# Performance work log

Hardware: AMD Instinct MI355X
Metric: run time of the kernel (lower is better)

Reference implementation:

```python
import jax, jax.numpy as jnp
import numpy as np

RADIUS = 0.1
NSAMPLE = 32
EPS = 1e-5


def ball_query(radius, nsample, xyz):
    # xyz: [B, N, 3] -> idx [B, N, nsample] (query set == support set)
    B, N, _ = xyz.shape
    # pairwise squared distances [B, N, N]
    sq = jnp.sum((xyz[:, :, None, :] - xyz[:, None, :, :]) ** 2, axis=-1)
    grp = jnp.broadcast_to(jnp.arange(N, dtype=jnp.int32), (B, N, N))
    grp = jnp.where(sq > radius * radius, N, grp)
    grp = jnp.sort(grp, axis=-1)[:, :, :nsample]
    first = grp[:, :, 0:1]
    return jnp.where(grp == N, first, grp)  # self is always in-ball -> first valid


def index_points(points, idx):
    # points [B, N, C], idx [B, N, S] -> [B, N, S, C]
    B, N, S = idx.shape
    C = points.shape[-1]
    flat = jnp.take_along_axis(points, idx.reshape(B, N * S, 1), axis=1)
    return flat.reshape(B, N, S, C)


def bn(x, gamma, beta, mean, var, axis):
    # eval-mode batchnorm over channel axis
    shape = [1] * x.ndim
    shape[axis] = -1
    g = gamma.reshape(shape); b = beta.reshape(shape)
    m = mean.reshape(shape); v = var.reshape(shape)
    return (x - m) * (g * jax.lax.rsqrt(v + EPS)) + b


def setup_inputs() -> dict:
    key = jax.random.key(0)
    ks = jax.random.split(key, 8)
    B, N, C, E = 4, 4096, 128, 4
    H = C * E
    xyz = jax.random.uniform(ks[0], (B, N, 3), dtype=jnp.float32)
    feats = jax.random.normal(ks[1], (B, N, C), dtype=jnp.float32)
    s = 0.05
    Wn = jax.random.normal(ks[2], (C, C + 3), dtype=jnp.float32) * s
    W1 = jax.random.normal(ks[3], (H, C), dtype=jnp.float32) * s
    W2 = jax.random.normal(ks[4], (C, H), dtype=jnp.float32) * s
    def bnp(k, n):
        k1, k2 = jax.random.split(k)
        return (jnp.ones((n,), jnp.float32) + 0.01 * jax.random.normal(k1, (n,)),
                0.01 * jax.random.normal(k2, (n,)),
                jnp.zeros((n,), jnp.float32),
                jnp.ones((n,), jnp.float32))
    gn, bn_, mn, vn = bnp(ks[5], C)
    g1, b1, m1, v1 = bnp(ks[6], H)
    g2, b2, m2, v2 = bnp(ks[7], C)
    return dict(xyz=xyz, feats=feats, Wn=Wn, gn=gn, bn_=bn_, mn=mn, vn=vn,
                W1=W1, g1=g1, b1=b1, m1=m1, v1=v1,
                W2=W2, g2=g2, b2=b2, m2=m2, v2=v2)


def reference(xyz, feats, Wn, gn, bn_, mn, vn, W1, g1, b1, m1, v1, W2, g2, b2, m2, v2):
    B, N, C = feats.shape
    identity = feats  # [B, N, C]
    idx = ball_query(RADIUS, NSAMPLE, xyz)  # [B, N, S]
    grouped_xyz = index_points(xyz, idx) - xyz[:, :, None, :]  # [B, N, S, 3]
    grouped_xyz = grouped_xyz / RADIUS  # normalize_dp
    grouped_feats = index_points(feats, idx)  # [B, N, S, C]
    grouped = jnp.concatenate([grouped_xyz, grouped_feats], axis=-1)  # [B, N, S, C+3]
    # torch layout [B, C+3, S, N]; keep [B, N, S, C+3] and contract channels
    x = jnp.einsum('oc,bnsc->bnso', Wn, grouped)  # neighbor 1x1 conv
    x = jax.nn.relu(bn(x, gn, bn_, mn, vn, axis=3))
    x = jnp.max(x, axis=2)  # max over neighbors -> [B, N, C]
    # inverted bottleneck pointwise MLP
    h = jnp.einsum('hc,bnc->bnh', W1, x)
    h = jax.nn.relu(bn(h, g1, b1, m1, v1, axis=2))
    y = jnp.einsum('ch,bnh->bnc', W2, h)
    y = bn(y, g2, b2, m2, v2, axis=2)
    out = jax.nn.relu(y + identity)  # [B, N, C]
    return out
```

## Files before the change

### kernel.cpp

```cpp
#include <hip/hip_runtime.h>
#include <hip/hip_bf16.h>
#include <math.h>

static constexpr int BB = 4;
static constexpr int NN = 4096;
static constexpr int CC = 128;
static constexpr int HH = 512;
static constexpr int SS = 32;
static constexpr float EPSF = 1e-5f;
static constexpr int NCELL = 1000;

typedef __bf16 bf16_t;
typedef bf16_t bf16x8 __attribute__((ext_vector_type(8)));
typedef float f32x4 __attribute__((ext_vector_type(4)));
typedef float f32x2 __attribute__((ext_vector_type(2)));

__device__ inline unsigned short f2bf(float f) {
    unsigned int u = __builtin_bit_cast(unsigned int, f);
    u += 0x7FFFu + ((u >> 16) & 1u);
    return (unsigned short)(u >> 16);
}
__device__ inline float bf2f(unsigned short s) {
    unsigned int u = ((unsigned int)s) << 16;
    return __builtin_bit_cast(float, u);
}
__device__ inline float u2f(unsigned int u) {
    return __builtin_bit_cast(float, u);
}
__device__ inline int cell_of(float v) {
    int c = (int)(v * 10.0f);
    return c > 9 ? 9 : (c < 0 ? 0 : c);
}
__device__ inline f32x2 pk_fma_b(f32x2 a, float g, f32x2 c) {
    const f32x2 gg = {g, g};
    return a * gg + c;
}

__device__ inline void gload_lds16(const void* g, void* l) {
    __builtin_amdgcn_global_load_lds(
        (const __attribute__((address_space(1))) unsigned int*)g,
        (__attribute__((address_space(3))) unsigned int*)l, 16, 0, 0);
}

__global__ __launch_bounds__(256)
void prep_kernel(const float* __restrict__ Wn, const float* __restrict__ W1,
                 const float* __restrict__ W2, const float* __restrict__ feats,
                 const float* __restrict__ gn, const float* __restrict__ bnv,
                 const float* __restrict__ mn, const float* __restrict__ vn,
                 unsigned short* __restrict__ WnF, unsigned short* __restrict__ W1b,
                 unsigned short* __restrict__ W2b, unsigned short* __restrict__ featsb,
                 int* __restrict__ counts, float4* __restrict__ wfold)
{
    const int blk = blockIdx.x;
    const int t   = threadIdx.x;
    if (blk < 576) {
        const int i = blk * 256 + t;
        if (i < 16384) {
            const int o = i >> 7, c = i & 127;
            WnF[i] = f2bf(Wn[o * 131 + 3 + c]);
        } else if (i < 16384 + 65536) {
            const int k = i - 16384;
            W1b[k] = f2bf(W1[k]);
        } else if (i < 16384 + 131072) {
            const int k = i - 16384 - 65536;
            W2b[k] = f2bf(W2[k]);
        }
    } else if (blk < 2624) {
        const int i = (blk - 576) * 256 + t;
        const float4 v = ((const float4*)feats)[i];
        unsigned long long pk = (unsigned long long)f2bf(v.x)
                              | ((unsigned long long)f2bf(v.y) << 16)
                              | ((unsigned long long)f2bf(v.z) << 32)
                              | ((unsigned long long)f2bf(v.w) << 48);
        ((unsigned long long*)featsb)[i] = pk;
    } else if (blk < 2640) {
        const int i = (blk - 2624) * 256 + t;
        if (i < BB * NCELL) counts[i] = 0;
    } else {
        if (t < CC) {
            const float sc = gn[t] / sqrtf(vn[t] + EPSF);
            wfold[t] = make_float4(sc * Wn[t * 131 + 0], sc * Wn[t * 131 + 1],
                                   sc * Wn[t * 131 + 2], bnv[t] - mn[t] * sc);
        }
    }
}

__global__ __launch_bounds__(256)
void count_kernel(const float* __restrict__ xyz, int* __restrict__ counts)
{
    const int p = blockIdx.x * 256 + threadIdx.x;
    const int b = p >> 12;
    const float x = xyz[p * 3 + 0], y = xyz[p * 3 + 1], z = xyz[p * 3 + 2];
    const int cid = cell_of(z) * 100 + cell_of(y) * 10 + cell_of(x);
    atomicAdd(&counts[b * NCELL + cid], 1);
}

__global__ __launch_bounds__(1024)
void scan_kernel(const int* __restrict__ counts, int* __restrict__ starts,
                 int* __restrict__ cursor)
{
    const int t  = threadIdx.x;
    const int i0 = t * 4;
    int v[4];
    #pragma unroll
    for (int k = 0; k < 4; ++k)
        v[k] = (i0 + k < BB * NCELL) ? counts[i0 + k] : 0;
    const int s = v[0] + v[1] + v[2] + v[3];

    __shared__ int ls[1024];
    ls[t] = s;
    __syncthreads();
    #pragma unroll
    for (int off = 1; off < 1024; off <<= 1) {
        const int add = (t >= off) ? ls[t - off] : 0;
        __syncthreads();
        ls[t] += add;
        __syncthreads();
    }
    int ex = ls[t] - s;
    #pragma unroll
    for (int k = 0; k < 4; ++k) {
        if (i0 + k < BB * NCELL) {
            starts[i0 + k] = ex;
            cursor[i0 + k] = ex;
        }
        ex += v[k];
    }
    if (t == 1023) starts[BB * NCELL] = ls[1023];
}

__global__ __launch_bounds__(256)
void scatter_kernel(const float* __restrict__ xyz, int* __restrict__ cursor,
                    float4* __restrict__ spts)
{
    const int p = blockIdx.x * 256 + threadIdx.x;
    const int b = p >> 12;
    const int n = p & (NN - 1);
    const float x = xyz[p * 3 + 0], y = xyz[p * 3 + 1], z = xyz[p * 3 + 2];
    const int cid = cell_of(z) * 100 + cell_of(y) * 10 + cell_of(x);
    const int pos = atomicAdd(&cursor[b * NCELL + cid], 1);
    spts[pos] = make_float4(x, y, z, __int_as_float(n));
}

__global__ __launch_bounds__(64)
void ball_query_binned_kernel(const float* __restrict__ xyz,
                              const int* __restrict__ starts,
                              const float4* __restrict__ spts,
                              int* __restrict__ idx)
{
    const int p    = blockIdx.x;
    const int b    = p >> 12;
    const int lane = threadIdx.x;

    const float qx = xyz[p * 3 + 0];
    const float qy = xyz[p * 3 + 1];
    const float qz = xyz[p * 3 + 2];
    const int cx = cell_of(qx), cy = cell_of(qy), cz = cell_of(qz);
    const int xlo = cx > 0 ? cx - 1 : 0;
    const int xhi = cx < 9 ? cx + 1 : 9;

    __shared__ int list[128];
    __shared__ int res[SS];
    int cnt = 0;

    for (int dz = -1; dz <= 1; ++dz) {
        const int z2 = cz + dz;
        if (z2 < 0 || z2 > 9) continue;
        for (int dy = -1; dy <= 1; ++dy) {
            const int y2 = cy + dy;
            if (y2 < 0 || y2 > 9) continue;
            const int base = b * NCELL + z2 * 100 + y2 * 10;
            const int lo = starts[base + xlo];
            const int hi = starts[base + xhi + 1];
            for (int j0 = lo; j0 < hi; j0 += 64) {
                const int j = j0 + lane;
                bool in = false;
                int pi = 0;
                if (j < hi) {
                    const float4 s = spts[j];
                    float sq;
                    {
                        #pragma clang fp contract(off)
                        const float dx  = qx - s.x;
                        const float dyv = qy - s.y;
                        const float dzv = qz - s.z;
                        sq = dx * dx + dyv * dyv + dzv * dzv;
                    }
                    in = (sq <= 0.01f);
                    pi = __float_as_int(s.w);
                }
                const unsigned long long mask = __ballot(in);
                if (in) {
                    const int pos = cnt + __popcll(mask & ((1ull << lane) - 1ull));
                    if (pos < 128) list[pos] = pi;
                }
                cnt += (int)__popcll(mask);
            }
        }
    }
    __syncthreads();

    const int c = cnt < 128 ? cnt : 128;
    #pragma unroll
    for (int l0 = 0; l0 < 2; ++l0) {
        const int l = lane + l0 * 64;
        if (l < c) {
            const int v = list[l];
            int r = 0;
            for (int k = 0; k < c; ++k) r += (list[k] < v);
            if (r < SS) res[r] = v;
        }
    }
    __syncthreads();

    if (lane < SS) {
        const int m = c < SS ? c : SS;
        idx[(size_t)p * SS + lane] = (lane < m) ? res[lane] : res[0];
    }
}

__global__ __launch_bounds__(256)
void group_max_kernel(const float* __restrict__ xyz,
                      const unsigned short* __restrict__ T,
                      const float4* __restrict__ wfold,
                      const int* __restrict__ idx, unsigned short* __restrict__ xout)
{
    const int t   = threadIdx.x;
    const int ptl = t >> 5;
    const int l   = t & 31;
    const int p   = blockIdx.x * 8 + ptl;
    const int b   = p >> 12;

    __shared__ float4 sg[8][32];

    {
        const int j = idx[(size_t)p * SS + l];
        const float* q  = xyz + (size_t)p * 3;
        const float* pj = xyz + ((size_t)b * NN + j) * 3;
        sg[ptl][l] = make_float4((pj[0] - q[0]) / 0.1f,
                                 (pj[1] - q[1]) / 0.1f,
                                 (pj[2] - q[2]) / 0.1f, __int_as_float(j));
    }
    __syncthreads();

    const int c0 = l * 4;
    const float4 wa = wfold[c0 + 0], wb = wfold[c0 + 1];
    const float4 wc = wfold[c0 + 2], wd = wfold[c0 + 3];
    const f32x2 w0p0 = {wa.x, wb.x}, w1p0 = {wa.y, wb.y}, w2p0 = {wa.z, wb.z};
    const f32x2 w0p1 = {wc.x, wd.x}, w1p1 = {wc.y, wd.y}, w2p1 = {wc.z, wd.z};

    const unsigned short* Tb = T + (size_t)b * NN * CC;
    f32x2 mx0 = {-1e30f, -1e30f}, mx1 = {-1e30f, -1e30f};

    #pragma unroll 8
    for (int s = 0; s < SS; ++s) {
        const float4 g = sg[ptl][s];
        const int j = __float_as_int(g.w);
        const uint2 tv = *(const uint2*)(Tb + (size_t)j * CC + c0);
        f32x2 v0, v1;
        v0.x = u2f(tv.x << 16); v0.y = u2f(tv.x & 0xFFFF0000u);
        v1.x = u2f(tv.y << 16); v1.y = u2f(tv.y & 0xFFFF0000u);
        v0 = pk_fma_b(w0p0, g.x, v0); v0 = pk_fma_b(w1p0, g.y, v0); v0 = pk_fma_b(w2p0, g.z, v0);
        v1 = pk_fma_b(w0p1, g.x, v1); v1 = pk_fma_b(w1p1, g.y, v1); v1 = pk_fma_b(w2p1, g.z, v1);
        mx0.x = fmaxf(mx0.x, v0.x); mx0.y = fmaxf(mx0.y, v0.y);
        mx1.x = fmaxf(mx1.x, v1.x); mx1.y = fmaxf(mx1.y, v1.y);
    }

    const float r0 = fmaxf(mx0.x + wa.w, 0.f);
    const float r1 = fmaxf(mx0.y + wb.w, 0.f);
    const float r2 = fmaxf(mx1.x + wc.w, 0.f);
    const float r3 = fmaxf(mx1.y + wd.w, 0.f);
    uint2 o;
    o.x = (unsigned)f2bf(r0) | ((unsigned)f2bf(r1) << 16);
    o.y = (unsigned)f2bf(r2) | ((unsigned)f2bf(r3) << 16);
    *(uint2*)(xout + (size_t)p * CC + c0) = o;
}

template<int MODE>
__global__ __launch_bounds__(256, 2)
void mfma_gemm_kernel(const unsigned short* __restrict__ A, const unsigned short* __restrict__ W,
                      const float* __restrict__ g, const float* __restrict__ bb,
                      const float* __restrict__ mu, const float* __restrict__ var,
                      const float* __restrict__ res, void* __restrict__ outv,
                      int M, int Nout, int K)
{
    constexpr int BM = 64, BN = 128, BK = 64;
    __shared__ char smem[(BM + BN) * BK * 2];
    char* sA = smem;
    char* sB = smem + BM * BK * 2;

    const int t    = threadIdx.x;
    const int lane = t & 63;
    const int w    = t >> 6;
    const int wm   = w >> 1;
    const int wn   = w & 1;
    const int m0   = blockIdx.x * BM;
    const int o0   = blockIdx.y * BN;
    const int Kb   = K * 2;

    f32x4 acc[2][4];
    #pragma unroll
    for (int i = 0; i < 2; ++i)
        #pragma unroll
        for (int j = 0; j < 4; ++j) acc[i][j] = f32x4{0.f, 0.f, 0.f, 0.f};

    const char* Ab = (const char*)A;
    const char* Wb = (const char*)W;

    for (int kc = 0; kc < K; kc += BK) {
        const int kcb = kc * 2;
        #pragma unroll
        for (int l = 0; l < 2; ++l) {
            const int q     = w * 2 + l;
            const int Lb    = q * 1024 + lane * 16;
            const int row   = Lb >> 7;
            const int inrow = Lb & 127;
            const char* src = Ab + (size_t)(m0 + row) * Kb + kcb + (inrow ^ ((row & 7) << 4));
            gload_lds16(src, sA + q * 1024);
        }
        #pragma unroll
        for (int l = 0; l < 4; ++l) {
            const int q     = w * 4 + l;
            const int Lb    = q * 1024 + lane * 16;
            const int row   = Lb >> 7;
            const int inrow = Lb & 127;
            const char* src = Wb + (size_t)(o0 + row) * Kb + kcb + (inrow ^ ((row & 7) << 4));
            gload_lds16(src, sB + q * 1024);
        }
        __syncthreads();

        #pragma unroll
        for (int ks = 0; ks < 2; ++ks) {
            const int kbyte = ks * 64 + (lane >> 4) * 16;
            bf16x8 af[2], bf[4];
            #pragma unroll
            for (int i = 0; i < 2; ++i) {
                const int r = wm * 32 + i * 16 + (lane & 15);
                af[i] = *(const bf16x8*)(sA + r * 128 + (kbyte ^ ((r & 7) << 4)));
            }
            #pragma unroll
            for (int j = 0; j < 4; ++j) {
                const int r = wn * 64 + j * 16 + (lane & 15);
                bf[j] = *(const bf16x8*)(sB + r * 128 + (kbyte ^ ((r & 7) << 4)));
            }
            #pragma unroll
            for (int i = 0; i < 2; ++i)
                #pragma unroll
                for (int j = 0; j < 4; ++j)
                    acc[i][j] = __builtin_amdgcn_mfma_f32_16x16x32_bf16(af[i], bf[j], acc[i][j], 0, 0, 0);
        }
        __syncthreads();
    }

    #pragma unroll
    for (int j = 0; j < 4; ++j) {
        const int col = o0 + wn * 64 + j * 16 + (lane & 15);
        float scg = 1.f, sh = 0.f, mm = 0.f;
        if constexpr (MODE == 1 || MODE == 2) {
            scg = g[col] / sqrtf(var[col] + EPSF);
            mm  = mu[col];
            sh  = bb[col];
        }
        if constexpr (MODE == 3) {
            scg = g[col] / sqrtf(var[col] + EPSF);
        }
        #pragma unroll
        for (int i = 0; i < 2; ++i) {
            const int rowb = m0 + wm * 32 + i * 16 + (lane >> 4) * 4;
            #pragma unroll
            for (int r = 0; r < 4; ++r) {
                float z = acc[i][j][r];
                if constexpr (MODE == 1 || MODE == 2) z = (z - mm) * scg + sh;
                if constexpr (MODE == 3) z = z * scg;
                if constexpr (MODE == 2) z += res[(size_t)(rowb + r) * Nout + col];
                if constexpr (MODE == 1 || MODE == 2) z = fmaxf(z, 0.f);
                if constexpr (MODE == 2)
                    ((float*)outv)[(size_t)(rowb + r) * Nout + col] = z;
                else
                    ((unsigned short*)outv)[(size_t)(rowb + r) * Nout + col] = f2bf(z);
            }
        }
    }
}

extern "C" void kernel_launch(void* const* d_in, const int* in_sizes, int n_in,
                              void* d_out, int out_size, void* d_ws, size_t ws_size,
                              hipStream_t stream)
{
    const float* xyz   = (const float*)d_in[0];
    const float* feats = (const float*)d_in[1];
    const float* Wn    = (const float*)d_in[2];
    const float* gn    = (const float*)d_in[3];
    const float* bn_   = (const float*)d_in[4];
    const float* mn    = (const float*)d_in[5];
    const float* vn    = (const float*)d_in[6];
    const float* W1    = (const float*)d_in[7];
    const float* g1    = (const float*)d_in[8];
    const float* b1    = (const float*)d_in[9];
    const float* m1    = (const float*)d_in[10];
    const float* v1    = (const float*)d_in[11];
    const float* W2    = (const float*)d_in[12];
    const float* g2    = (const float*)d_in[13];
    const float* b2    = (const float*)d_in[14];
    const float* m2    = (const float*)d_in[15];
    const float* v2    = (const float*)d_in[16];
    float* out = (float*)d_out;

    char* ws = (char*)d_ws;
    int*            idx    = (int*)(ws);
    int*            counts = (int*)(ws + 2097152);
    int*            starts = (int*)(ws + 2113536);
    int*            cursor = (int*)(ws + 2129920);
    float4*         spts   = (float4*)(ws + 2146304);
    unsigned short* WnF    = (unsigned short*)(ws +  2408448);
    unsigned short* W1b    = (unsigned short*)(ws +  2441216);
    unsigned short* W2b    = (unsigned short*)(ws +  2572288);
    unsigned short* featsb = (unsigned short*)(ws +  2703360);
    unsigned short* Tb     = (unsigned short*)(ws +  6897664);
    unsigned short* xb     = (unsigned short*)(ws + 11091968);
    unsigned short* hb     = (unsigned short*)(ws + 15286272);
    float4*         wfold  = (float4*)(ws + 32063488);

    const int M = BB * NN;

    prep_kernel<<<2641, 256, 0, stream>>>(Wn, W1, W2, feats, gn, bn_, mn, vn,
                                          WnF, W1b, W2b, featsb, counts, wfold);
    count_kernel<<<64, 256, 0, stream>>>(xyz, counts);
    scan_kernel<<<1, 1024, 0, stream>>>(counts, starts, cursor);
    scatter_kernel<<<64, 256, 0, stream>>>(xyz, cursor, spts);
    ball_query_binned_kernel<<<M, 64, 0, stream>>>(xyz, starts, spts, idx);

    mfma_gemm_kernel<3><<<dim3(M / 64, 1), 256, 0, stream>>>(
        featsb, WnF, gn, nullptr, nullptr, vn, nullptr, Tb, M, CC, CC);

    group_max_kernel<<<M / 8, 256, 0, stream>>>(xyz, Tb, wfold, idx, xb);

    mfma_gemm_kernel<1><<<dim3(M / 64, HH / 128), 256, 0, stream>>>(
        xb, W1b, g1, b1, m1, v1, nullptr, hb, M, HH, CC);

    mfma_gemm_kernel<2><<<dim3(M / 64, 1), 256, 0, stream>>>(
        hb, W2b, g2, b2, m2, v2, feats, out, M, CC, HH);
}
```

Before: 159.1 us.

## Fuse binning into one per-batch kernel, convert feats in GEMM, split final GEMM

Replaces the count, scan and scatter kernels and the global counts/cursor buffers with a single per-batch block that bins points using shared-memory atomics and a local scan. It drops the separate fp32-to-bf16 conversion of feats: the first GEMM now loads fp32 feats and converts them while staging into LDS. It also adds a template N-tile width and runs the final GEMM with 64-wide tiles over two column blocks to raise block count. These changes cut kernel launches and an intermediate buffer. In exchange, binning now runs on only four blocks, and the A operand of the first GEMM uses plain loads instead of direct-to-LDS loads.

```diff
diff --git a/kernel.cpp b/kernel.cpp
--- a/kernel.cpp
+++ b/kernel.cpp
@@ -20,10 +20,6 @@
     u += 0x7FFFu + ((u >> 16) & 1u);
     return (unsigned short)(u >> 16);
 }
-__device__ inline float bf2f(unsigned short s) {
-    unsigned int u = ((unsigned int)s) << 16;
-    return __builtin_bit_cast(float, u);
-}
 __device__ inline float u2f(unsigned int u) {
     return __builtin_bit_cast(float, u);
 }
@@ -44,12 +40,11 @@
 
 __global__ __launch_bounds__(256)
 void prep_kernel(const float* __restrict__ Wn, const float* __restrict__ W1,
-                 const float* __restrict__ W2, const float* __restrict__ feats,
+                 const float* __restrict__ W2,
                  const float* __restrict__ gn, const float* __restrict__ bnv,
                  const float* __restrict__ mn, const float* __restrict__ vn,
                  unsigned short* __restrict__ WnF, unsigned short* __restrict__ W1b,
-                 unsigned short* __restrict__ W2b, unsigned short* __restrict__ featsb,
-                 int* __restrict__ counts, float4* __restrict__ wfold)
+                 unsigned short* __restrict__ W2b, float4* __restrict__ wfold)
 {
     const int blk = blockIdx.x;
     const int t   = threadIdx.x;
@@ -65,17 +60,6 @@
             const int k = i - 16384 - 65536;
             W2b[k] = f2bf(W2[k]);
         }
-    } else if (blk < 2624) {
-        const int i = (blk - 576) * 256 + t;
-        const float4 v = ((const float4*)feats)[i];
-        unsigned long long pk = (unsigned long long)f2bf(v.x)
-                              | ((unsigned long long)f2bf(v.y) << 16)
-                              | ((unsigned long long)f2bf(v.z) << 32)
-                              | ((unsigned long long)f2bf(v.w) << 48);
-        ((unsigned long long*)featsb)[i] = pk;
-    } else if (blk < 2640) {
-        const int i = (blk - 2624) * 256 + t;
-        if (i < BB * NCELL) counts[i] = 0;
     } else {
         if (t < CC) {
             const float sc = gn[t] / sqrtf(vn[t] + EPSF);
@@ -85,30 +69,35 @@
     }
 }
 
-__global__ __launch_bounds__(256)
-void count_kernel(const float* __restrict__ xyz, int* __restrict__ counts)
-{
-    const int p = blockIdx.x * 256 + threadIdx.x;
-    const int b = p >> 12;
-    const float x = xyz[p * 3 + 0], y = xyz[p * 3 + 1], z = xyz[p * 3 + 2];
-    const int cid = cell_of(z) * 100 + cell_of(y) * 10 + cell_of(x);
-    atomicAdd(&counts[b * NCELL + cid], 1);
-}
-
 __global__ __launch_bounds__(1024)
-void scan_kernel(const int* __restrict__ counts, int* __restrict__ starts,
-                 int* __restrict__ cursor)
-{
-    const int t  = threadIdx.x;
-    const int i0 = t * 4;
-    int v[4];
-    #pragma unroll
-    for (int k = 0; k < 4; ++k)
-        v[k] = (i0 + k < BB * NCELL) ? counts[i0 + k] : 0;
-    const int s = v[0] + v[1] + v[2] + v[3];
-
+void bin_kernel(const float* __restrict__ xyz, int* __restrict__ starts,
+                float4* __restrict__ spts)
+{
+    const int b = blockIdx.x;
+    const int t = threadIdx.x;
+
+    __shared__ int cur[1024];
     __shared__ int ls[1024];
-    ls[t] = s;
+
+    cur[t] = 0;
+    __syncthreads();
+
+    int    cid[4];
+    float4 pt[4];
+    #pragma unroll
+    for (int k = 0; k < 4; ++k) {
+        const int n = k * 1024 + t;
+        const float x = xyz[((size_t)b * NN + n) * 3 + 0];
+        const float y = xyz[((size_t)b * NN + n) * 3 + 1];
+        const float z = xyz[((size_t)b * NN + n) * 3 + 2];
+        cid[k] = cell_of(z) * 100 + cell_of(y) * 10 + cell_of(x);
+        pt[k]  = make_float4(x, y, z, __int_as_float(n));
+        atomicAdd(&cur[cid[k]], 1);
+    }
+    __syncthreads();
+
+    const int v = cur[t];
+    ls[t] = v;
     __syncthreads();
     #pragma unroll
     for (int off = 1; off < 1024; off <<= 1) {
@@ -117,29 +106,18 @@
         ls[t] += add;
         __syncthreads();
     }
-    int ex = ls[t] - s;
+    const int ex = ls[t] - v;
+    if (t < NCELL) starts[b * NCELL + t] = b * NN + ex;
+    if (b == 0 && t == 0) starts[BB * NCELL] = BB * NN;
+    __syncthreads();
+    cur[t] = ex;
+    __syncthreads();
+
     #pragma unroll
     for (int k = 0; k < 4; ++k) {
-        if (i0 + k < BB * NCELL) {
-            starts[i0 + k] = ex;
-            cursor[i0 + k] = ex;
-        }
-        ex += v[k];
-    }
-    if (t == 1023) starts[BB * NCELL] = ls[1023];
-}
-
-__global__ __launch_bounds__(256)
-void scatter_kernel(const float* __restrict__ xyz, int* __restrict__ cursor,
-                    float4* __restrict__ spts)
-{
-    const int p = blockIdx.x * 256 + threadIdx.x;
-    const int b = p >> 12;
-    const int n = p & (NN - 1);
-    const float x = xyz[p * 3 + 0], y = xyz[p * 3 + 1], z = xyz[p * 3 + 2];
-    const int cid = cell_of(z) * 100 + cell_of(y) * 10 + cell_of(x);
-    const int pos = atomicAdd(&cursor[b * NCELL + cid], 1);
-    spts[pos] = make_float4(x, y, z, __int_as_float(n));
+        const int pos = atomicAdd(&cur[cid[k]], 1);
+        spts[(size_t)b * NN + pos] = pt[k];
+    }
 }
 
 __global__ __launch_bounds__(64)
@@ -276,7 +254,7 @@
     *(uint2*)(xout + (size_t)p * CC + c0) = o;
 }
 
-template<int MODE>
+template<int MODE, int BNt>
 __global__ __launch_bounds__(256, 2)
 void mfma_gemm_kernel(const unsigned short* __restrict__ A, const unsigned short* __restrict__ W,
                       const float* __restrict__ g, const float* __restrict__ bb,
@@ -284,8 +262,9 @@
                       const float* __restrict__ res, void* __restrict__ outv,
                       int M, int Nout, int K)
 {
-    constexpr int BM = 64, BN = 128, BK = 64;
-    __shared__ char smem[(BM + BN) * BK * 2];
+    constexpr int BM = 64, BK = 64;
+    constexpr int NF = BNt / 32;
+    __shared__ char smem[(BM + BNt) * BK * 2];
     char* sA = smem;
     char* sB = smem + BM * BK * 2;
 
@@ -295,16 +274,17 @@
     const int wm   = w >> 1;
     const int wn   = w & 1;
     const int m0   = blockIdx.x * BM;
-    const int o0   = blockIdx.y * BN;
+    const int o0   = blockIdx.y * BNt;
     const int Kb   = K * 2;
 
-    f32x4 acc[2][4];
+    f32x4 acc[2][NF];
     #pragma unroll
     for (int i = 0; i < 2; ++i)
         #pragma unroll
-        for (int j = 0; j < 4; ++j) acc[i][j] = f32x4{0.f, 0.f, 0.f, 0.f};
+        for (int j = 0; j < NF; ++j) acc[i][j] = f32x4{0.f, 0.f, 0.f, 0.f};
 
     const char* Ab = (const char*)A;
+    const float* Af = (const float*)A;
     const char* Wb = (const char*)W;
 
     for (int kc = 0; kc < K; kc += BK) {
@@ -315,12 +295,25 @@
             const int Lb    = q * 1024 + lane * 16;
             const int row   = Lb >> 7;
             const int inrow = Lb & 127;
-            const char* src = Ab + (size_t)(m0 + row) * Kb + kcb + (inrow ^ ((row & 7) << 4));
-            gload_lds16(src, sA + q * 1024);
+            const int sw    = inrow ^ ((row & 7) << 4);
+            if constexpr (MODE == 3) {
+                const float* src = Af + (size_t)(m0 + row) * K + kc + (sw >> 1);
+                const float4 a0 = *(const float4*)(src);
+                const float4 a1 = *(const float4*)(src + 4);
+                uint4 pk;
+                pk.x = (unsigned)f2bf(a0.x) | ((unsigned)f2bf(a0.y) << 16);
+                pk.y = (unsigned)f2bf(a0.z) | ((unsigned)f2bf(a0.w) << 16);
+                pk.z = (unsigned)f2bf(a1.x) | ((unsigned)f2bf(a1.y) << 16);
+                pk.w = (unsigned)f2bf(a1.z) | ((unsigned)f2bf(a1.w) << 16);
+                *(uint4*)(sA + Lb) = pk;
+            } else {
+                const char* src = Ab + (size_t)(m0 + row) * Kb + kcb + sw;
+                gload_lds16(src, sA + q * 1024);
+            }
         }
         #pragma unroll
-        for (int l = 0; l < 4; ++l) {
-            const int q     = w * 4 + l;
+        for (int l = 0; l < NF; ++l) {
+            const int q     = w * NF + l;
             const int Lb    = q * 1024 + lane * 16;
             const int row   = Lb >> 7;
             const int inrow = Lb & 127;
@@ -332,29 +325,29 @@
         #pragma unroll
         for (int ks = 0; ks < 2; ++ks) {
             const int kbyte = ks * 64 + (lane >> 4) * 16;
-            bf16x8 af[2], bf[4];
+            bf16x8 af[2], bf[NF];
             #pragma unroll
             for (int i = 0; i < 2; ++i) {
                 const int r = wm * 32 + i * 16 + (lane & 15);
                 af[i] = *(const bf16x8*)(sA + r * 128 + (kbyte ^ ((r & 7) << 4)));
             }
             #pragma unroll
-            for (int j = 0; j < 4; ++j) {
-                const int r = wn * 64 + j * 16 + (lane & 15);
+            for (int j = 0; j < NF; ++j) {
+                const int r = wn * (BNt / 2) + j * 16 + (lane & 15);
                 bf[j] = *(const bf16x8*)(sB + r * 128 + (kbyte ^ ((r & 7) << 4)));
             }
             #pragma unroll
             for (int i = 0; i < 2; ++i)
                 #pragma unroll
-                for (int j = 0; j < 4; ++j)
+                for (int j = 0; j < NF; ++j)
                     acc[i][j] = __builtin_amdgcn_mfma_f32_16x16x32_bf16(af[i], bf[j], acc[i][j], 0, 0, 0);
         }
         __syncthreads();
     }
 
     #pragma unroll
-    for (int j = 0; j < 4; ++j) {
-        const int col = o0 + wn * 64 + j * 16 + (lane & 15);
+    for (int j = 0; j < NF; ++j) {
+        const int col = o0 + wn * (BNt / 2) + j * 16 + (lane & 15);
         float scg = 1.f, sh = 0.f, mm = 0.f;
         if constexpr (MODE == 1 || MODE == 2) {
             scg = g[col] / sqrtf(var[col] + EPSF);
@@ -408,36 +401,31 @@
 
     char* ws = (char*)d_ws;
     int*            idx    = (int*)(ws);
-    int*            counts = (int*)(ws + 2097152);
-    int*            starts = (int*)(ws + 2113536);
-    int*            cursor = (int*)(ws + 2129920);
-    float4*         spts   = (float4*)(ws + 2146304);
-    unsigned short* WnF    = (unsigned short*)(ws +  2408448);
-    unsigned short* W1b    = (unsigned short*)(ws +  2441216);
-    unsigned short* W2b    = (unsigned short*)(ws +  2572288);
-    unsigned short* featsb = (unsigned short*)(ws +  2703360);
-    unsigned short* Tb     = (unsigned short*)(ws +  6897664);
-    unsigned short* xb     = (unsigned short*)(ws + 11091968);
-    unsigned short* hb     = (unsigned short*)(ws + 15286272);
-    float4*         wfold  = (float4*)(ws + 32063488);
+    int*            starts = (int*)(ws + 2097152);
+    float4*         spts   = (float4*)(ws + 2113536);
+    unsigned short* WnF    = (unsigned short*)(ws + 2375680);
+    unsigned short* W1b    = (unsigned short*)(ws + 2408448);
+    unsigned short* W2b    = (unsigned short*)(ws + 2539520);
+    unsigned short* Tb     = (unsigned short*)(ws + 2670592);
+    unsigned short* xb     = (unsigned short*)(ws + 6864896);
+    unsigned short* hb     = (unsigned short*)(ws + 11059200);
+    float4*         wfold  = (float4*)(ws + 27836416);
 
     const int M = BB * NN;
 
-    prep_kernel<<<2641, 256, 0, stream>>>(Wn, W1, W2, feats, gn, bn_, mn, vn,
-                                          WnF, W1b, W2b, featsb, counts, wfold);
-    count_kernel<<<64, 256, 0, stream>>>(xyz, counts);
-    scan_kernel<<<1, 1024, 0, stream>>>(counts, starts, cursor);
-    scatter_kernel<<<64, 256, 0, stream>>>(xyz, cursor, spts);
+    prep_kernel<<<577, 256, 0, stream>>>(Wn, W1, W2, gn, bn_, mn, vn,
+                                         WnF, W1b, W2b, wfold);
+    bin_kernel<<<BB, 1024, 0, stream>>>(xyz, starts, spts);
     ball_query_binned_kernel<<<M, 64, 0, stream>>>(xyz, starts, spts, idx);
 
-    mfma_gemm_kernel<3><<<dim3(M / 64, 1), 256, 0, stream>>>(
-        featsb, WnF, gn, nullptr, nullptr, vn, nullptr, Tb, M, CC, CC);
+    mfma_gemm_kernel<3, 128><<<dim3(M / 64, 1), 256, 0, stream>>>(
+        (const unsigned short*)feats, WnF, gn, nullptr, nullptr, vn, nullptr, Tb, M, CC, CC);
 
     group_max_kernel<<<M / 8, 256, 0, stream>>>(xyz, Tb, wfold, idx, xb);
 
-    mfma_gemm_kernel<1><<<dim3(M / 64, HH / 128), 256, 0, stream>>>(
+    mfma_gemm_kernel<1, 128><<<dim3(M / 64, HH / 128), 256, 0, stream>>>(
         xb, W1b, g1, b1, m1, v1, nullptr, hb, M, HH, CC);
 
-    mfma_gemm_kernel<2><<<dim3(M / 64, 1), 256, 0, stream>>>(
+    mfma_gemm_kernel<2, 64><<<dim3(M / 64, CC / 64), 256, 0, stream>>>(
         hb, W2b, g2, b2, m2, v2, feats, out, M, CC, HH);
 }
```

New measurement: 155.9 us. 1.02x faster.
